# Performance work log

Hardware: AMD Instinct MI355X
Metric: run time of the kernel (lower is better)

The kernel has to match this reference:

```python
import jax, jax.numpy as jnp
import numpy as np
from jax import lax

N_SAMPLES = 2048
RADIUS = 0.2
K_GROUP = 32
BN_EPS = 1e-5


def furthest_point_sampling(xyz, n_samples):
    # xyz: [B, N, 3] -> indices [B, n_samples] (start from index 0)
    B, N, _ = xyz.shape

    def body(carry, _):
        dists, last = carry                                   # [B,N], [B]
        cur = jnp.take_along_axis(xyz, last[:, None, None], axis=1)  # [B,1,3]
        d = jnp.sum((xyz - cur) ** 2, axis=-1)                # [B,N]
        dists = jnp.minimum(dists, d)
        nxt = jnp.argmax(dists, axis=-1).astype(jnp.int32)    # [B]
        return (dists, nxt), nxt

    init = (jnp.full((B, N), 1e10, xyz.dtype), jnp.zeros((B,), jnp.int32))
    _, idxs = lax.scan(body, init, None, length=n_samples - 1)  # [n_samples-1, B]
    return jnp.concatenate([jnp.zeros((1, B), jnp.int32), idxs], axis=0).T  # [B,n_samples]


def ball_query(xyz, centroids, radius, k):
    # xyz: [B,N,3], centroids: [B,S,3] -> [B,S,k] neighbor indices within radius
    N = xyz.shape[1]
    d2 = jnp.sum((centroids[:, :, None, :] - xyz[:, None, :, :]) ** 2, axis=-1)  # [B,S,N]
    cand = jnp.where(d2 <= radius * radius, jnp.arange(N, dtype=jnp.int32), N)   # invalid -> N
    neg_topk, _ = lax.top_k(-cand, k)        # k smallest indices, ascending
    idx = -neg_topk                          # [B,S,k]
    first = idx[:, :, :1]                    # pad slots beyond valid count with first neighbor
    return jnp.where(idx == N, first, idx)


def batch_gather(data, idx):
    # data: [B,N,C], idx: [B,...] -> [B,...,C]
    return jax.vmap(lambda d, i: d[i])(data, idx)


def setup_inputs() -> dict:
    key = jax.random.key(0)
    ks = jax.random.split(key, 16)
    B, N, F = 8, 8192, 64
    inp = {
        "points_xyz": jax.random.uniform(ks[0], (B, N, 3), jnp.float32),
        "features": jax.random.normal(ks[1], (B, N, F), jnp.float32),
    }
    chans = [67, 64, 64, 128]
    for i in range(3):
        cin, cout = chans[i], chans[i + 1]
        scale = 1.0 / np.sqrt(cin)
        inp[f"w{i}"] = jax.random.uniform(ks[2 + 4 * i], (cout, cin), jnp.float32, -scale, scale)
        inp[f"b{i}"] = jax.random.uniform(ks[3 + 4 * i], (cout,), jnp.float32, -scale, scale)
        inp[f"g{i}"] = jnp.ones((cout,), jnp.float32)
        inp[f"beta{i}"] = jnp.zeros((cout,), jnp.float32)
    return inp


def reference(points_xyz, features, w0, b0, g0, beta0, w1, b1, g1, beta1, w2, b2, g2, beta2):
    B = points_xyz.shape[0]
    centroid_idx = furthest_point_sampling(points_xyz, N_SAMPLES)          # [B,S]
    centroids = jnp.take_along_axis(points_xyz, centroid_idx[:, :, None], axis=1)  # [B,S,3]
    grouped_idx = ball_query(points_xyz, centroids, RADIUS, K_GROUP)       # [B,S,K]
    grouped_xyz = batch_gather(points_xyz, grouped_idx)                    # [B,S,K,3]
    grouped_feat = batch_gather(features, grouped_idx)                     # [B,S,K,F]
    grouped_xyz_norm = grouped_xyz - centroids[:, :, None, :]
    x = jnp.concatenate([grouped_xyz_norm, grouped_feat], axis=-1)         # [B,S,K,C]

    for w, b, g, bt in ((w0, b0, g0, beta0), (w1, b1, g1, beta1), (w2, b2, g2, beta2)):
        x = jnp.einsum("bskc,oc->bsko", x, w) + b                          # 1x1 conv
        mean = jnp.mean(x, axis=(0, 1, 2))                                 # BN (train-mode batch stats)
        var = jnp.var(x, axis=(0, 1, 2))
        x = jax.nn.relu(g * (x - mean) * lax.rsqrt(var + BN_EPS) + bt)

    out = jnp.max(x, axis=2)                                               # max over group -> [B,S,Cout]
    return centroids, out
```

## Files before the change

kernel.cpp:

```cpp
#include <hip/hip_runtime.h>
#include <cstdint>
#include <cstddef>

#define NPTS 8192
#define NB 8
#define NS 2048
#define KG 32
#define NROWS (NB*NS*KG)
#define NREP 32

__device__ __forceinline__ float dist2_exact(float ax, float ay, float az,
                                             float bx, float by, float bz)
{
#pragma clang fp contract(off)
  float dx = ax - bx;
  float dy = ay - by;
  float dz = az - bz;
  return dx * dx + dy * dy + dz * dz;
}

__device__ __forceinline__ unsigned mort3(unsigned v) {
  return (v & 1u) | ((v & 2u) << 2) | ((v & 4u) << 4);
}

__launch_bounds__(256)
__global__ void sort_kernel(const float* __restrict__ xyz,
                            float* __restrict__ sX, float* __restrict__ sY,
                            float* __restrict__ sZ, unsigned* __restrict__ sO)
{
  __shared__ unsigned hist[512];
  __shared__ unsigned startv[512];
  __shared__ unsigned short cellid[NPTS];
  const int b = blockIdx.x, t = threadIdx.x;
  const float* base = xyz + (size_t)b * NPTS * 3;

  for (int q = t; q < 512; q += 256) hist[q] = 0u;
  __syncthreads();
  for (int q = t; q < NPTS; q += 256) {
    float x = base[3*q], y = base[3*q+1], z = base[3*q+2];
    int ix = (int)(x * 8.f); ix = ix < 0 ? 0 : (ix > 7 ? 7 : ix);
    int iy = (int)(y * 8.f); iy = iy < 0 ? 0 : (iy > 7 ? 7 : iy);
    int iz = (int)(z * 8.f); iz = iz < 0 ? 0 : (iz > 7 ? 7 : iz);
    unsigned m = mort3((unsigned)ix) | (mort3((unsigned)iy) << 1) | (mort3((unsigned)iz) << 2);
    cellid[q] = (unsigned short)m;
    atomicAdd(&hist[m], 1u);
  }
  __syncthreads();
  if (t == 0) {
    unsigned run = 0;
    for (int i = 0; i < 512; ++i) { unsigned h = hist[i]; startv[i] = run; run += h; }
  }
  __syncthreads();
  for (int q = t; q < NPTS; q += 256) {
    unsigned m = cellid[q];
    unsigned pos = atomicAdd(&startv[m], 1u);
    size_t o = (size_t)b * NPTS + pos;
    sX[o] = base[3*q]; sY[o] = base[3*q+1]; sZ[o] = base[3*q+2];
    sO[o] = (unsigned)q;
  }
}

__launch_bounds__(512)
__global__ void fps_kernel(const float* __restrict__ sX, const float* __restrict__ sY,
                           const float* __restrict__ sZ, const unsigned* __restrict__ sO,
                           const float* __restrict__ xyz, float* __restrict__ cents)
{
  __shared__ float sx[NPTS], sy[NPTS], sz[NPTS];
  __shared__ float scent[NS * 3];
  __shared__ unsigned long long spk[2][8];

  const int b = blockIdx.x;
  const int t = threadIdx.x;
  const int w = t >> 6, lane = t & 63;
  const size_t sb = (size_t)b * NPTS;

  float px[16], py[16], pz[16], dmin[16];
  unsigned lo[16];
#pragma unroll
  for (int j = 0; j < 16; ++j) {
    int i = w * 1024 + j * 64 + lane;
    float x = sX[sb + i], y = sY[sb + i], z = sZ[sb + i];
    px[j] = x; py[j] = y; pz[j] = z;
    dmin[j] = 1e10f;
    lo[j] = ~((sO[sb + i] << 13) | (unsigned)i);
    sx[i] = x; sy[i] = y; sz[i] = z;
  }
  float bxl = px[0], bxh = px[0], byl = py[0], byh = py[0], bzl = pz[0], bzh = pz[0];
#pragma unroll
  for (int j = 1; j < 16; ++j) {
    bxl = fminf(bxl, px[j]); bxh = fmaxf(bxh, px[j]);
    byl = fminf(byl, py[j]); byh = fmaxf(byh, py[j]);
    bzl = fminf(bzl, pz[j]); bzh = fmaxf(bzh, pz[j]);
  }
#pragma unroll
  for (int off = 1; off <= 32; off <<= 1) {
    bxl = fminf(bxl, __shfl_xor(bxl, off, 64)); bxh = fmaxf(bxh, __shfl_xor(bxh, off, 64));
    byl = fminf(byl, __shfl_xor(byl, off, 64)); byh = fmaxf(byh, __shfl_xor(byh, off, 64));
    bzl = fminf(bzl, __shfl_xor(bzl, off, 64)); bzh = fmaxf(bzh, __shfl_xor(bzh, off, 64));
  }

  unsigned long long bestc = ((unsigned long long)__float_as_uint(1e10f) << 32);

  const float* o0 = xyz + sb * 3;
  float cx = o0[0], cy = o0[1], cz = o0[2];
  if (t == 0) { scent[0] = cx; scent[1] = cy; scent[2] = cz; }
  __syncthreads();

  for (int it = 1; it < NS; ++it) {
    float qx = cx - fminf(fmaxf(cx, bxl), bxh);
    float qy = cy - fminf(fmaxf(cy, byl), byh);
    float qz = cz - fminf(fmaxf(cz, bzl), bzh);
    float dbox2 = (qx*qx + qy*qy + qz*qz) * 0.999f;
    float tmaxw = __uint_as_float((unsigned)(bestc >> 32));
    if (dbox2 < tmaxw) {
      float bm = -1.0f;
      unsigned lb = 0u;
#pragma unroll
      for (int j = 0; j < 16; ++j) {
        float d = dist2_exact(px[j], py[j], pz[j], cx, cy, cz);
        float m = fminf(dmin[j], d);
        dmin[j] = m;
        bool take = (m > bm);
        bm = take ? m : bm;
        lb = take ? lo[j] : lb;
      }
      unsigned long long best = ((unsigned long long)__float_as_uint(bm) << 32)
                              | (unsigned long long)lb;
#pragma unroll
      for (int off = 32; off > 0; off >>= 1) {
        unsigned long long op = __shfl_xor(best, off, 64);
        best = (op > best) ? op : best;
      }
      bestc = best;
    }
    const int pb = it & 1;
    if (lane == 0) spk[pb][w] = bestc;
    __syncthreads();
    unsigned long long bb = spk[pb][0];
#pragma unroll
    for (int q = 1; q < 8; ++q) {
      unsigned long long oq = spk[pb][q];
      bb = (oq > bb) ? oq : bb;
    }
    const int win = (int)((~(unsigned)bb) & 8191u);
    cx = sx[win]; cy = sy[win]; cz = sz[win];
    if (t == 0) { scent[3*it] = cx; scent[3*it+1] = cy; scent[3*it+2] = cz; }
  }
  __syncthreads();
  float* cb = cents + (size_t)b * NS * 3;
  for (int q = t; q < NS * 3; q += 512) cb[q] = scent[q];
}

__launch_bounds__(256)
__global__ void ballq_kernel(const float* __restrict__ xyz,
                             const float* __restrict__ cents,
                             int* __restrict__ gidx)
{
  const int gid  = blockIdx.x * 256 + threadIdx.x;
  const int w    = gid >> 6;
  const int lane = gid & 63;
  const int b    = w >> 11;
  const float* base = xyz + (size_t)b * NPTS * 3;
  const float cx = cents[3*w+0], cy = cents[3*w+1], cz = cents[3*w+2];
  const float R2 = (float)(0.2 * 0.2);
  int* out = gidx + (size_t)w * KG;

  int filled = 0, first = -1;
  for (int c = 0; c < NPTS/64; ++c) {
    int i = (c << 6) | lane;
    float d = dist2_exact(base[3*i+0], base[3*i+1], base[3*i+2], cx, cy, cz);
    bool inb = (d <= R2);
    unsigned long long mask = __ballot(inb);
    if (first < 0 && mask) first = (c << 6) + (__ffsll((long long)mask) - 1);
    int pre  = __popcll(mask & ((1ull << lane) - 1ull));
    int slot = filled + pre;
    if (inb && slot < KG) out[slot] = i;
    filled += __popcll(mask);
    if (filled >= KG) break;
  }
  if (filled < KG && lane < KG && lane >= filled) out[lane] = first;
}

template<int H>
__device__ __forceinline__ void fold_sum_step(float* a, int lane) {
#pragma unroll
  for (int q = 0; q < H; ++q) {
    float keep = (lane & H) ? a[q + H] : a[q];
    float send = (lane & H) ? a[q] : a[q + H];
    a[q] = keep + __shfl_xor(send, H, 64);
  }
}

__device__ __forceinline__ float fold_sum16(float* a, int lane) {
  fold_sum_step<8>(a, lane);
  fold_sum_step<4>(a, lane);
  fold_sum_step<2>(a, lane);
  fold_sum_step<1>(a, lane);
  float v = a[0];
  v += __shfl_xor(v, 16, 64);
  v += __shfl_xor(v, 32, 64);
  return v;
}

template<int H>
__device__ __forceinline__ void fold_max_step(float* a, int lane) {
#pragma unroll
  for (int q = 0; q < H; ++q) {
    float keep = (lane & H) ? a[q + H] : a[q];
    float send = (lane & H) ? a[q] : a[q + H];
    a[q] = fmaxf(keep, __shfl_xor(send, H, 64));
  }
}

__device__ __forceinline__ float fold_max16(float* a, int lane) {
  fold_max_step<8>(a, lane);
  fold_max_step<4>(a, lane);
  fold_max_step<2>(a, lane);
  fold_max_step<1>(a, lane);
  float v = a[0];
  v = fmaxf(v, __shfl_xor(v, 16, 64));
  return v;
}

template<int H>
__device__ __forceinline__ void fold_min_step(float* a, int lane) {
#pragma unroll
  for (int q = 0; q < H; ++q) {
    float keep = (lane & H) ? a[q + H] : a[q];
    float send = (lane & H) ? a[q] : a[q + H];
    a[q] = fminf(keep, __shfl_xor(send, H, 64));
  }
}

__device__ __forceinline__ float fold_min16(float* a, int lane) {
  fold_min_step<8>(a, lane);
  fold_min_step<4>(a, lane);
  fold_min_step<2>(a, lane);
  fold_min_step<1>(a, lane);
  float v = a[0];
  v = fminf(v, __shfl_xor(v, 16, 64));
  return v;
}

__device__ __forceinline__ void stats16(float* y, int lane, int o0,
                                        float* __restrict__ gs1,
                                        float* __restrict__ gs2)
{
  float sq[16];
#pragma unroll
  for (int q = 0; q < 16; ++q) sq[q] = y[q] * y[q];
  float s1 = fold_sum16(y, lane);
  float s2 = fold_sum16(sq, lane);
  if (lane < 16)       atomicAdd(&gs1[o0 + lane], s1);
  else if (lane < 32)  atomicAdd(&gs2[o0 + (lane & 15)], s2);
}

__device__ __forceinline__ void minmax16(const float* y, int lane, int o0, int cs,
                                         float* __restrict__ zmax,
                                         float* __restrict__ zmin)
{
  float ymx[16], ymn[16];
#pragma unroll
  for (int q = 0; q < 16; ++q) { ymx[q] = y[q]; ymn[q] = y[q]; }
  float mx = fold_max16(ymx, lane);
  float mn = fold_min16(ymn, lane);
  if (!(lane & 16)) {
    zmax[(size_t)cs * 128 + o0 + (lane & 15)] = mx;
    zmin[(size_t)cs * 128 + o0 + (lane & 15)] = mn;
  }
}

__device__ __forceinline__ unsigned short f2b(float f) {
  unsigned b = __float_as_uint(f);
  return (unsigned short)((b + 0x7FFFu + ((b >> 16) & 1u)) >> 16);
}
__device__ __forceinline__ float b2f(unsigned short h) {
  return __uint_as_float(((unsigned)h) << 16);
}

__launch_bounds__(256, 3)
__global__ void k1_kernel(const float* __restrict__ xyz, const float* __restrict__ feats,
                          const float* __restrict__ cents, const int* __restrict__ gidx,
                          const float* __restrict__ w0, const float* __restrict__ b0,
                          float* __restrict__ stats, unsigned short* __restrict__ actL)
{
  const int t = threadIdx.x, lane = t & 63;
  const int r = blockIdx.x * 256 + t;
  const int b = r >> 16, cs = r >> 5;
  const int i = gidx[r];
  const int rep = (blockIdx.x * 4 + (t >> 6)) & (NREP - 1);
  const float* pp = xyz + ((size_t)(b << 13) + i) * 3;
  const float* cc = cents + (size_t)cs * 3;
  const float* fb = feats + (((size_t)(b << 13) + i) << 6);

  float xin[67];
  xin[0] = pp[0] - cc[0]; xin[1] = pp[1] - cc[1]; xin[2] = pp[2] - cc[2];
  const float4* f4 = (const float4*)fb;
#pragma unroll
  for (int q = 0; q < 16; ++q) {
    float4 v = f4[q];
    xin[3+4*q+0] = v.x; xin[3+4*q+1] = v.y; xin[3+4*q+2] = v.z; xin[3+4*q+3] = v.w;
  }

  for (int o0 = 0; o0 < 64; o0 += 16) {
    float y[16];
#pragma unroll
    for (int k = 0; k < 16; ++k) {
      float a = b0[o0 + k];
#pragma unroll
      for (int c = 0; c < 67; ++c)
        a = fmaf(w0[(o0 + k)*67 + c], xin[c], a);
      y[k] = a;
    }
#pragma unroll
    for (int k = 0; k < 16; ++k)
      actL[(size_t)(o0 + k) * NROWS + r] = f2b(y[k]);
    stats16(y, lane, o0, stats + (size_t)rep*64, stats + 2048 + (size_t)rep*64);
  }
}

__launch_bounds__(256, 3)
__global__ void k2_kernel(unsigned short* __restrict__ actL,
                          const float* __restrict__ w1, const float* __restrict__ b1,
                          const float* __restrict__ prm,
                          float* __restrict__ stats)
{
  const int t = threadIdx.x, lane = t & 63;
  const int r = blockIdx.x * 256 + t;
  const int rep = (blockIdx.x * 4 + (t >> 6)) & (NREP - 1);

  float x[64];
#pragma unroll
  for (int c = 0; c < 64; ++c)
    x[c] = b2f(actL[(size_t)c * NROWS + r]);
#pragma unroll
  for (int c = 0; c < 64; ++c)
    x[c] = fmaxf(fmaf(prm[c], x[c], prm[64 + c]), 0.f);

  for (int o0 = 0; o0 < 64; o0 += 16) {
    float y[16];
#pragma unroll
    for (int k = 0; k < 16; ++k) {
      float a = b1[o0 + k];
#pragma unroll
      for (int c = 0; c < 64; ++c)
        a = fmaf(w1[(o0 + k)*64 + c], x[c], a);
      y[k] = a;
    }
#pragma unroll
    for (int k = 0; k < 16; ++k)
      actL[(size_t)(o0 + k) * NROWS + r] = f2b(y[k]);
    stats16(y, lane, o0, stats + 4096 + (size_t)rep*64, stats + 6144 + (size_t)rep*64);
  }
}

__launch_bounds__(256, 3)
__global__ void k3_kernel(const unsigned short* __restrict__ actL,
                          const float* __restrict__ w2, const float* __restrict__ b2,
                          const float* __restrict__ prm,
                          float* __restrict__ stats,
                          float* __restrict__ zmax, float* __restrict__ zmin)
{
  const int t = threadIdx.x, lane = t & 63;
  const int r = blockIdx.x * 256 + t;
  const int cs = r >> 5;
  const int rep = (blockIdx.x * 4 + (t >> 6)) & (NREP - 1);

  float x[64];
#pragma unroll
  for (int c = 0; c < 64; ++c)
    x[c] = b2f(actL[(size_t)c * NROWS + r]);
#pragma unroll
  for (int c = 0; c < 64; ++c)
    x[c] = fmaxf(fmaf(prm[128 + c], x[c], prm[192 + c]), 0.f);

  for (int o0 = 0; o0 < 128; o0 += 16) {
    float y[16];
#pragma unroll
    for (int k = 0; k < 16; ++k) {
      float a = b2[o0 + k];
#pragma unroll
      for (int c = 0; c < 64; ++c)
        a = fmaf(w2[(o0 + k)*64 + c], x[c], a);
      y[k] = a;
    }
    minmax16(y, lane, o0, cs, zmax, zmin);
    stats16(y, lane, o0, stats + 8192 + (size_t)rep*128, stats + 12288 + (size_t)rep*128);
  }
}

__launch_bounds__(256)
__global__ void outfin_kernel(const float* __restrict__ zmax,
                              const float* __restrict__ zmin,
                              const float* __restrict__ prm,
                              float* __restrict__ outp)
{
  int i = blockIdx.x * 256 + threadIdx.x;
  int ch = i & 127;
  float a = prm[256 + ch], sh = prm[384 + ch];
  float z = (a >= 0.f) ? zmax[i] : zmin[i];
  outp[i] = fmaxf(fmaf(a, z, sh), 0.f);
}

template<int MODE>
__launch_bounds__(256, (MODE <= 2 ? 4 : 2))
__global__ void chain_kernel(const float* __restrict__ xyz,
                             const float* __restrict__ feats,
                             const float* __restrict__ cents,
                             const int* __restrict__ gidx,
                             const float* __restrict__ w0, const float* __restrict__ b0,
                             const float* __restrict__ w1, const float* __restrict__ b1,
                             const float* __restrict__ w2, const float* __restrict__ b2,
                             const float* __restrict__ prm,
                             float* __restrict__ stats,
                             float* __restrict__ outp,
                             float* __restrict__ zmax, float* __restrict__ zmin)
{
  const int t    = threadIdx.x;
  const int lane = t & 63;
  const int r    = blockIdx.x * 256 + t;
  const int b    = r >> 16;
  const int cs   = r >> 5;
  const int i    = gidx[r];
  const int rep  = (blockIdx.x * 4 + (t >> 6)) & (NREP - 1);

  const float* pp = xyz + ((size_t)(b << 13) + i) * 3;
  const float* cc = cents + (size_t)cs * 3;
  const float* fb = feats + (((size_t)(b << 13) + i) << 6);

  float acc[64];
  {
    float c0 = pp[0] - cc[0], c1 = pp[1] - cc[1], c2 = pp[2] - cc[2];
#pragma unroll
    for (int o = 0; o < 64; ++o)
      acc[o] = fmaf(w0[o*67+2], c2, fmaf(w0[o*67+1], c1, fmaf(w0[o*67+0], c0, b0[o])));
  }
  for (int c0 = 0; c0 < 64; c0 += 16) {
    float xc[16];
    const float4* f4 = (const float4*)(fb + c0);
    float4 v0 = f4[0], v1 = f4[1], v2 = f4[2], v3 = f4[3];
    xc[0]=v0.x; xc[1]=v0.y; xc[2]=v0.z; xc[3]=v0.w;
    xc[4]=v1.x; xc[5]=v1.y; xc[6]=v1.z; xc[7]=v1.w;
    xc[8]=v2.x; xc[9]=v2.y; xc[10]=v2.z; xc[11]=v2.w;
    xc[12]=v3.x; xc[13]=v3.y; xc[14]=v3.z; xc[15]=v3.w;
#pragma unroll
    for (int o = 0; o < 64; ++o) {
      float a = acc[o];
#pragma unroll
      for (int ci = 0; ci < 16; ++ci)
        a = fmaf(w0[o*67 + 3 + c0 + ci], xc[ci], a);
      acc[o] = a;
    }
  }

  if (MODE == 1) {
#pragma unroll
    for (int o0 = 0; o0 < 64; o0 += 16) {
      float y[16];
#pragma unroll
      for (int q = 0; q < 16; ++q) y[q] = acc[o0 + q];
      stats16(y, lane, o0, stats + (size_t)rep*64, stats + 2048 + (size_t)rep*64);
    }
    return;
  }

#pragma unroll
  for (int o = 0; o < 64; ++o)
    acc[o] = fmaxf(fmaf(prm[o], acc[o], prm[64 + o]), 0.f);

  if (MODE == 2) {
    for (int o0 = 0; o0 < 64; o0 += 16) {
      float y[16];
#pragma unroll
      for (int k = 0; k < 16; ++k) {
        float a = b1[o0 + k];
#pragma unroll
        for (int c = 0; c < 64; ++c)
          a = fmaf(w1[(o0 + k)*64 + c], acc[c], a);
        y[k] = a;
      }
      stats16(y, lane, o0, stats + 4096 + (size_t)rep*64, stats + 6144 + (size_t)rep*64);
    }
    return;
  }

  float y1[64];
#pragma unroll
  for (int o = 0; o < 64; ++o) {
    float a = b1[o];
#pragma unroll
    for (int c = 0; c < 64; ++c)
      a = fmaf(w1[o*64 + c], acc[c], a);
    y1[o] = a;
  }
#pragma unroll
  for (int o = 0; o < 64; ++o)
    y1[o] = fmaxf(fmaf(prm[128 + o], y1[o], prm[192 + o]), 0.f);

  if (MODE == 3 || MODE == 5) {
    for (int o0 = 0; o0 < 128; o0 += 16) {
      float y[16];
#pragma unroll
      for (int k = 0; k < 16; ++k) {
        float a = b2[o0 + k];
#pragma unroll
        for (int c = 0; c < 64; ++c)
          a = fmaf(w2[(o0 + k)*64 + c], y1[c], a);
        y[k] = a;
      }
      if (MODE == 5) minmax16(y, lane, o0, cs, zmax, zmin);
      stats16(y, lane, o0, stats + 8192 + (size_t)rep*128, stats + 12288 + (size_t)rep*128);
    }
    return;
  }

  for (int o0 = 0; o0 < 128; o0 += 16) {
    float y[16];
#pragma unroll
    for (int k = 0; k < 16; ++k) {
      float a = b2[o0 + k];
#pragma unroll
      for (int c = 0; c < 64; ++c)
        a = fmaf(w2[(o0 + k)*64 + c], y1[c], a);
      y[k] = a;
    }
#pragma unroll
    for (int k = 0; k < 16; ++k)
      y[k] = fmaxf(fmaf(prm[256 + o0 + k], y[k], prm[384 + o0 + k]), 0.f);
    float m = fold_max16(y, lane);
    if (!(lane & 16))
      outp[(size_t)cs * 128 + o0 + (lane & 15)] = m;
  }
}

__global__ void finalize_kernel(const float* __restrict__ stats,
                                const float* __restrict__ g,
                                const float* __restrict__ beta,
                                float* __restrict__ pa, float* __restrict__ psh, int C)
{
  int c = threadIdx.x;
  if (c >= C) return;
  float s1 = 0.f, s2 = 0.f;
  for (int rr = 0; rr < NREP; ++rr) { s1 += stats[rr*C + c]; s2 += stats[NREP*C + rr*C + c]; }
  const float invn = 1.0f / (float)NROWS;
  float mean = s1 * invn;
  float var  = s2 * invn - mean * mean;
  float rs   = 1.0f / sqrtf(var + 1e-5f);
  float a    = g[c] * rs;
  pa[c]  = a;
  psh[c] = fmaf(-mean, a, beta[c]);
}

__global__ void zero_kernel(float* __restrict__ p, int n)
{
  int i = blockIdx.x * 256 + threadIdx.x;
  if (i < n) p[i] = 0.f;
}

extern "C" void kernel_launch(void* const* d_in, const int* in_sizes, int n_in,
                              void* d_out, int out_size, void* d_ws, size_t ws_size,
                              hipStream_t stream)
{
  (void)in_sizes; (void)n_in; (void)out_size;
  const float* xyz   = (const float*)d_in[0];
  const float* feats = (const float*)d_in[1];
  const float* w0 = (const float*)d_in[2],  *b0 = (const float*)d_in[3];
  const float* g0 = (const float*)d_in[4],  *bt0 = (const float*)d_in[5];
  const float* w1 = (const float*)d_in[6],  *b1 = (const float*)d_in[7];
  const float* g1 = (const float*)d_in[8],  *bt1 = (const float*)d_in[9];
  const float* w2 = (const float*)d_in[10], *b2 = (const float*)d_in[11];
  const float* g2 = (const float*)d_in[12], *bt2 = (const float*)d_in[13];

  float* cents = (float*)d_out;
  float* outp  = cents + (size_t)NB * NS * 3;

  char* wsb = (char*)d_ws;
  int*   gidx  = (int*)wsb;
  float* stats = (float*)(wsb + (2ull << 20));
  float* prm   = stats + 16384;
  float* sX = (float*)(wsb + (2ull << 20) + (512u << 10));
  float* sY = sX + (size_t)NB * NPTS;
  float* sZ = sY + (size_t)NB * NPTS;
  unsigned* sO = (unsigned*)(sZ + (size_t)NB * NPTS);
  float* zmax  = (float*)(wsb + (4ull  << 20));
  float* zmin  = (float*)(wsb + (12ull << 20));
  unsigned short* actL = (unsigned short*)(wsb + (20ull << 20));
  const size_t need_A = (20ull << 20) + (size_t)NROWS * 64 * 2;
  const size_t need_B = (20ull << 20);

  zero_kernel<<<64, 256, 0, stream>>>(stats, 16384);
  sort_kernel<<<NB, 256, 0, stream>>>(xyz, sX, sY, sZ, sO);
  fps_kernel<<<NB, 512, 0, stream>>>(sX, sY, sZ, sO, xyz, cents);
  ballq_kernel<<<(NB*NS*64)/256, 256, 0, stream>>>(xyz, cents, gidx);

  if (ws_size >= need_A) {
    k1_kernel<<<NROWS/256, 256, 0, stream>>>(xyz, feats, cents, gidx, w0, b0, stats, actL);
    finalize_kernel<<<1, 128, 0, stream>>>(stats + 0, g0, bt0, prm + 0, prm + 64, 64);
    k2_kernel<<<NROWS/256, 256, 0, stream>>>(actL, w1, b1, prm, stats);
    finalize_kernel<<<1, 128, 0, stream>>>(stats + 4096, g1, bt1, prm + 128, prm + 192, 64);
    k3_kernel<<<NROWS/256, 256, 0, stream>>>(actL, w2, b2, prm, stats, zmax, zmin);
    finalize_kernel<<<1, 128, 0, stream>>>(stats + 8192, g2, bt2, prm + 256, prm + 384, 128);
    outfin_kernel<<<(16384*128)/256, 256, 0, stream>>>(zmax, zmin, prm, outp);
  } else if (ws_size >= need_B) {
    chain_kernel<1><<<NROWS/256, 256, 0, stream>>>(xyz, feats, cents, gidx,
        w0, b0, w1, b1, w2, b2, prm, stats, outp, zmax, zmin);
    finalize_kernel<<<1, 128, 0, stream>>>(stats + 0, g0, bt0, prm + 0, prm + 64, 64);
    chain_kernel<2><<<NROWS/256, 256, 0, stream>>>(xyz, feats, cents, gidx,
        w0, b0, w1, b1, w2, b2, prm, stats, outp, zmax, zmin);
    finalize_kernel<<<1, 128, 0, stream>>>(stats + 4096, g1, bt1, prm + 128, prm + 192, 64);
    chain_kernel<5><<<NROWS/256, 256, 0, stream>>>(xyz, feats, cents, gidx,
        w0, b0, w1, b1, w2, b2, prm, stats, outp, zmax, zmin);
    finalize_kernel<<<1, 128, 0, stream>>>(stats + 8192, g2, bt2, prm + 256, prm + 384, 128);
    outfin_kernel<<<(16384*128)/256, 256, 0, stream>>>(zmax, zmin, prm, outp);
  } else {
    chain_kernel<1><<<NROWS/256, 256, 0, stream>>>(xyz, feats, cents, gidx,
        w0, b0, w1, b1, w2, b2, prm, stats, outp, zmax, zmin);
    finalize_kernel<<<1, 128, 0, stream>>>(stats + 0, g0, bt0, prm + 0, prm + 64, 64);
    chain_kernel<2><<<NROWS/256, 256, 0, stream>>>(xyz, feats, cents, gidx,
        w0, b0, w1, b1, w2, b2, prm, stats, outp, zmax, zmin);
    finalize_kernel<<<1, 128, 0, stream>>>(stats + 4096, g1, bt1, prm + 128, prm + 192, 64);
    chain_kernel<3><<<NROWS/256, 256, 0, stream>>>(xyz, feats, cents, gidx,
        w0, b0, w1, b1, w2, b2, prm, stats, outp, zmax, zmin);
    finalize_kernel<<<1, 128, 0, stream>>>(stats + 8192, g2, bt2, prm + 256, prm + 384, 128);
    chain_kernel<4><<<NROWS/256, 256, 0, stream>>>(xyz, feats, cents, gidx,
        w0, b0, w1, b1, w2, b2, prm, stats, outp, zmax, zmin);
  }
}
```

Measured before the change: 2.535 ms.

## Widen FPS blocks to 1024 threads and use DPP wave reductions

The furthest-point-sampling kernel now runs 1024 threads per batch, so each thread holds 8 points instead of 16 and the serial per-iteration distance update gets shorter. The per-thread argmax packs distance and index into one 64-bit key. The wave reduction uses DPP row operations plus readlane in place of shuffle-xor. The cross-wave step reads 16 partials in a tree. The aim is to cut latency on the 2047-step sequential loop, at the cost of more waves joining each block barrier. The per-wave bounding-box culling becomes finer as well.

```diff
diff --git a/kernel.cpp b/kernel.cpp
--- a/kernel.cpp
+++ b/kernel.cpp
@@ -21,6 +21,15 @@
 
 __device__ __forceinline__ unsigned mort3(unsigned v) {
   return (v & 1u) | ((v & 2u) << 2) | ((v & 4u) << 4);
+}
+
+template<int CTRL>
+__device__ __forceinline__ unsigned long long dpp_max_u64(unsigned long long v) {
+  int hi = (int)(unsigned)(v >> 32), lo = (int)(unsigned)v;
+  int h2 = __builtin_amdgcn_update_dpp(hi, hi, CTRL, 0xF, 0xF, false);
+  int l2 = __builtin_amdgcn_update_dpp(lo, lo, CTRL, 0xF, 0xF, false);
+  unsigned long long o = ((unsigned long long)(unsigned)h2 << 32) | (unsigned)l2;
+  return (o > v) ? o : v;
 }
 
 __launch_bounds__(256)
@@ -60,25 +69,25 @@
   }
 }
 
-__launch_bounds__(512)
+__launch_bounds__(1024)
 __global__ void fps_kernel(const float* __restrict__ sX, const float* __restrict__ sY,
                            const float* __restrict__ sZ, const unsigned* __restrict__ sO,
                            const float* __restrict__ xyz, float* __restrict__ cents)
 {
   __shared__ float sx[NPTS], sy[NPTS], sz[NPTS];
   __shared__ float scent[NS * 3];
-  __shared__ unsigned long long spk[2][8];
+  __shared__ unsigned long long spk[2][16];
 
   const int b = blockIdx.x;
   const int t = threadIdx.x;
   const int w = t >> 6, lane = t & 63;
   const size_t sb = (size_t)b * NPTS;
 
-  float px[16], py[16], pz[16], dmin[16];
-  unsigned lo[16];
-#pragma unroll
-  for (int j = 0; j < 16; ++j) {
-    int i = w * 1024 + j * 64 + lane;
+  float px[8], py[8], pz[8], dmin[8];
+  unsigned lo[8];
+#pragma unroll
+  for (int j = 0; j < 8; ++j) {
+    int i = w * 512 + j * 64 + lane;
     float x = sX[sb + i], y = sY[sb + i], z = sZ[sb + i];
     px[j] = x; py[j] = y; pz[j] = z;
     dmin[j] = 1e10f;
@@ -87,7 +96,7 @@
   }
   float bxl = px[0], bxh = px[0], byl = py[0], byh = py[0], bzl = pz[0], bzh = pz[0];
 #pragma unroll
-  for (int j = 1; j < 16; ++j) {
+  for (int j = 1; j < 8; ++j) {
     bxl = fminf(bxl, px[j]); bxh = fmaxf(bxh, px[j]);
     byl = fminf(byl, py[j]); byh = fmaxf(byh, py[j]);
     bzl = fminf(bzl, pz[j]); bzh = fmaxf(bzh, pz[j]);
@@ -113,42 +122,44 @@
     float dbox2 = (qx*qx + qy*qy + qz*qz) * 0.999f;
     float tmaxw = __uint_as_float((unsigned)(bestc >> 32));
     if (dbox2 < tmaxw) {
-      float bm = -1.0f;
-      unsigned lb = 0u;
-#pragma unroll
-      for (int j = 0; j < 16; ++j) {
+      unsigned long long best = 0ull;
+#pragma unroll
+      for (int j = 0; j < 8; ++j) {
         float d = dist2_exact(px[j], py[j], pz[j], cx, cy, cz);
         float m = fminf(dmin[j], d);
         dmin[j] = m;
-        bool take = (m > bm);
-        bm = take ? m : bm;
-        lb = take ? lo[j] : lb;
+        unsigned long long p = ((unsigned long long)__float_as_uint(m) << 32)
+                             | (unsigned long long)lo[j];
+        best = (p > best) ? p : best;
       }
-      unsigned long long best = ((unsigned long long)__float_as_uint(bm) << 32)
-                              | (unsigned long long)lb;
-#pragma unroll
-      for (int off = 32; off > 0; off >>= 1) {
-        unsigned long long op = __shfl_xor(best, off, 64);
-        best = (op > best) ? op : best;
-      }
-      bestc = best;
+      best = dpp_max_u64<0x111>(best);
+      best = dpp_max_u64<0x112>(best);
+      best = dpp_max_u64<0x114>(best);
+      best = dpp_max_u64<0x118>(best);
+      best = dpp_max_u64<0x142>(best);
+      best = dpp_max_u64<0x143>(best);
+      unsigned bh = (unsigned)__builtin_amdgcn_readlane((int)(unsigned)(best >> 32), 63);
+      unsigned bl = (unsigned)__builtin_amdgcn_readlane((int)(unsigned)best, 63);
+      bestc = ((unsigned long long)bh << 32) | bl;
     }
     const int pb = it & 1;
     if (lane == 0) spk[pb][w] = bestc;
     __syncthreads();
-    unsigned long long bb = spk[pb][0];
-#pragma unroll
-    for (int q = 1; q < 8; ++q) {
-      unsigned long long oq = spk[pb][q];
-      bb = (oq > bb) ? oq : bb;
-    }
-    const int win = (int)((~(unsigned)bb) & 8191u);
+    unsigned long long m[16];
+#pragma unroll
+    for (int q = 0; q < 16; ++q) m[q] = spk[pb][q];
+#pragma unroll
+    for (int s = 8; s > 0; s >>= 1)
+#pragma unroll
+      for (int q = 0; q < 8; ++q)
+        if (q < s) m[q] = (m[q + s] > m[q]) ? m[q + s] : m[q];
+    const int win = (int)((~(unsigned)m[0]) & 8191u);
     cx = sx[win]; cy = sy[win]; cz = sz[win];
     if (t == 0) { scent[3*it] = cx; scent[3*it+1] = cy; scent[3*it+2] = cz; }
   }
   __syncthreads();
   float* cb = cents + (size_t)b * NS * 3;
-  for (int q = t; q < NS * 3; q += 512) cb[q] = scent[q];
+  for (int q = t; q < NS * 3; q += 1024) cb[q] = scent[q];
 }
 
 __launch_bounds__(256)
@@ -590,7 +601,7 @@
 
   zero_kernel<<<64, 256, 0, stream>>>(stats, 16384);
   sort_kernel<<<NB, 256, 0, stream>>>(xyz, sX, sY, sZ, sO);
-  fps_kernel<<<NB, 512, 0, stream>>>(sX, sY, sZ, sO, xyz, cents);
+  fps_kernel<<<NB, 1024, 0, stream>>>(sX, sY, sZ, sO, xyz, cents);
   ballq_kernel<<<(NB*NS*64)/256, 256, 0, stream>>>(xyz, cents, gidx);
 
   if (ws_size >= need_A) {
```

Measured after the change: 2.575 ms. About the same (+1.6%).
